# Kernel tuning notes

Measured on AMD Instinct MI355X. Metric: run time of the kernel, lower is better.

Reference implementation:

```python
import jax, jax.numpy as jnp
import numpy as np

T, B, D, H, S = 512, 32, 1024, 1024, 512


def setup_inputs() -> dict:
    key = jax.random.key(0)
    ks = jax.random.split(key, 10)
    sc = 0.02
    return {
        "x": jax.random.normal(ks[0], (T, B, D), jnp.float32),
        "h0": jax.random.normal(ks[1], (B, H), jnp.float32),
        "c0": jax.random.normal(ks[2], (B, H), jnp.float32),
        "ctx": jax.random.normal(ks[3], (S, B, H), jnp.float32),
        # nn.Linear(input_size, 4*hidden_size) with bias
        "W_ih": jax.random.normal(ks[4], (4 * H, D), jnp.float32) * sc,
        "b_ih": jax.random.normal(ks[5], (4 * H,), jnp.float32) * sc,
        # nn.Linear(hidden_size, 4*hidden_size) with bias
        "W_hh": jax.random.normal(ks[6], (4 * H, H), jnp.float32) * sc,
        "b_hh": jax.random.normal(ks[7], (4 * H,), jnp.float32) * sc,
        # SoftDotAttention: linear_in (H->H, no bias), linear_out (2H->H, no bias)
        "W_in": jax.random.normal(ks[8], (H, H), jnp.float32) * sc,
        "W_out": jax.random.normal(ks[9], (H, 2 * H), jnp.float32) * sc,
    }


def reference(x, h0, c0, ctx, W_ih, b_ih, W_hh, b_hh, W_in, W_out):
    ctx_b = jnp.swapaxes(ctx, 0, 1)  # [B, S, H] (ctx.transpose(0,1))

    def step(carry, xt):
        hx, cx = carry
        gates = xt @ W_ih.T + b_ih + hx @ W_hh.T + b_hh  # [B, 4H]
        i, f, g, o = jnp.split(gates, 4, axis=1)
        cy = jax.nn.sigmoid(f) * cx + jax.nn.sigmoid(i) * jnp.tanh(g)
        hy = jax.nn.sigmoid(o) * jnp.tanh(cy)  # [B, H]
        # SoftDotAttention
        target = hy @ W_in.T  # [B, H]
        attn = jax.nn.softmax(jnp.einsum("bsh,bh->bs", ctx_b, target), axis=-1)
        wc = jnp.einsum("bs,bsh->bh", attn, ctx_b)  # weighted context
        h_tilde = jnp.tanh(jnp.concatenate([wc, hy], axis=1) @ W_out.T)
        return (h_tilde, cy), h_tilde

    (hT, cT), out = jax.lax.scan(step, (h0, c0), x)
    return out, hT, cT
```

## Files before the change

### kernel.cpp

```cpp
#include <hip/hip_runtime.h>
#include <hip/hip_bf16.h>
#include <cstdint>
#include <cstddef>

#define TT 512
#define BB 32
#define DD 1024
#define HH 1024
#define SS 512

typedef _Float16 f16x8 __attribute__((ext_vector_type(8)));
typedef _Float16 f16x4 __attribute__((ext_vector_type(4)));
typedef _Float16 f16x2 __attribute__((ext_vector_type(2)));
typedef float f32x4 __attribute__((ext_vector_type(4)));

__device__ __forceinline__ float sigm(float x) { return 1.0f / (1.0f + __expf(-x)); }
__device__ __forceinline__ float tanh_fast(float x) {
    return 1.0f - 2.0f / (__expf(2.0f * x) + 1.0f);
}
__device__ __forceinline__ f16x8 cvt8(const float* __restrict__ p) {
    float4 u = *(const float4*)p;
    float4 v = *(const float4*)(p + 4);
    f16x8 r;
    r[0] = (_Float16)u.x; r[1] = (_Float16)u.y; r[2] = (_Float16)u.z; r[3] = (_Float16)u.w;
    r[4] = (_Float16)v.x; r[5] = (_Float16)v.y; r[6] = (_Float16)v.z; r[7] = (_Float16)v.w;
    return r;
}

__device__ __forceinline__ void st_u32_coh(unsigned* p, unsigned v) {
    __hip_atomic_store(p, v, __ATOMIC_RELAXED, __HIP_MEMORY_SCOPE_AGENT);
}
__device__ __forceinline__ unsigned ld_u32_coh(const unsigned* p) {
    return __hip_atomic_load(p, __ATOMIC_RELAXED, __HIP_MEMORY_SCOPE_AGENT);
}
__device__ __forceinline__ unsigned long long ld_u64_coh(const unsigned long long* p) {
    return __hip_atomic_load(p, __ATOMIC_RELAXED, __HIP_MEMORY_SCOPE_AGENT);
}
__device__ __forceinline__ f16x8 ld16_coh(const _Float16* p) {
    union { unsigned long long q[2]; f16x8 h; } u;
    u.q[0] = ld_u64_coh((const unsigned long long*)p);
    u.q[1] = ld_u64_coh((const unsigned long long*)p + 1);
    return u.h;
}

__global__ __launch_bounds__(256) void k_cvt(const float* __restrict__ s,
                                             _Float16* __restrict__ d, int n4) {
    for (int i = blockIdx.x * blockDim.x + threadIdx.x; i < n4; i += gridDim.x * blockDim.x) {
        float4 v = ((const float4*)s)[i];
        f16x4 h;
        h[0] = (_Float16)v.x; h[1] = (_Float16)v.y;
        h[2] = (_Float16)v.z; h[3] = (_Float16)v.w;
        ((f16x4*)d)[i] = h;
    }
}

__global__ void k_bias(const float* __restrict__ bih, const float* __restrict__ bhh,
                       float* __restrict__ bsum) {
    const int i = blockIdx.x * blockDim.x + threadIdx.x;
    if (i < 4 * HH) bsum[i] = bih[i] + bhh[i];
}

__global__ void k_init(const float* __restrict__ c0, float* __restrict__ cbuf) {
    const int i = blockIdx.x * blockDim.x + threadIdx.x;
    if (i < BB * HH) cbuf[i] = c0[i];
}

__global__ void k_zero(unsigned* __restrict__ p) {
    const int i = blockIdx.x * blockDim.x + threadIdx.x;
    if (i < 1024) p[i] = 0u;
}

__global__ void k_fin(const float* __restrict__ lasth, const float* __restrict__ cbuf,
                      float* __restrict__ hT, float* __restrict__ cT) {
    const int i = blockIdx.x * blockDim.x + threadIdx.x;
    if (i < BB * HH) {
        hT[i] = lasth[i];
        cT[i] = cbuf[i];
    }
}

__global__ __launch_bounds__(256) void k_pre(const float* __restrict__ x,
                                             const float* __restrict__ Wih,
                                             _Float16* __restrict__ gx) {
    const int wave = (blockIdx.x * blockDim.x + threadIdx.x) >> 6;
    const int lane = threadIdx.x & 63;
    const int m0 = (wave >> 6) * 64, n0 = (wave & 63) * 64;
    const int lm = lane & 15, q8 = (lane >> 4) * 8;

    f32x4 acc[4][4];
    #pragma unroll
    for (int i = 0; i < 4; ++i)
        #pragma unroll
        for (int j = 0; j < 4; ++j) acc[i][j] = (f32x4)0.0f;

    for (int k0 = 0; k0 < DD; k0 += 32) {
        f16x8 a[4], b[4];
        #pragma unroll
        for (int i = 0; i < 4; ++i)
            a[i] = cvt8(x + (size_t)(m0 + i * 16 + lm) * DD + k0 + q8);
        #pragma unroll
        for (int j = 0; j < 4; ++j)
            b[j] = cvt8(Wih + (size_t)(n0 + j * 16 + lm) * DD + k0 + q8);
        #pragma unroll
        for (int i = 0; i < 4; ++i)
            #pragma unroll
            for (int j = 0; j < 4; ++j)
                acc[i][j] = __builtin_amdgcn_mfma_f32_16x16x32_f16(a[i], b[j], acc[i][j], 0, 0, 0);
    }
    const int rq = (lane >> 4) * 4;
    #pragma unroll
    for (int i = 0; i < 4; ++i)
        #pragma unroll
        for (int j = 0; j < 4; ++j)
            #pragma unroll
            for (int r = 0; r < 4; ++r)
                gx[(size_t)(m0 + i * 16 + rq + r) * (4 * HH) + n0 + j * 16 + lm] =
                    (_Float16)acc[i][j][r];
}

__global__ __launch_bounds__(256) void k_trwin(const float* __restrict__ Win,
                                               _Float16* __restrict__ WinT) {
    __shared__ float tile[32][33];
    const int bx = blockIdx.x & 31, by = blockIdx.x >> 5;
    const int tx = threadIdx.x & 31, ty = threadIdx.x >> 5;
    #pragma unroll
    for (int r = 0; r < 4; ++r)
        tile[ty + r * 8][tx] = Win[(size_t)(by * 32 + ty + r * 8) * HH + bx * 32 + tx];
    __syncthreads();
    #pragma unroll
    for (int r = 0; r < 4; ++r)
        WinT[(size_t)(bx * 32 + ty + r * 8) * HH + by * 32 + tx] =
            (_Float16)tile[tx][ty + r * 8];
}

__global__ __launch_bounds__(256) void k_ctxw(const float* __restrict__ ctxf,
                                              const _Float16* __restrict__ WinT,
                                              _Float16* __restrict__ ctxW) {
    const int wave = (blockIdx.x * blockDim.x + threadIdx.x) >> 6;
    const int lane = threadIdx.x & 63;
    const int m0 = (wave >> 4) * 64, n0 = (wave & 15) * 64;
    const int lm = lane & 15, q8 = (lane >> 4) * 8;

    f32x4 acc[4][4];
    #pragma unroll
    for (int i = 0; i < 4; ++i)
        #pragma unroll
        for (int j = 0; j < 4; ++j) acc[i][j] = (f32x4)0.0f;

    for (int k0 = 0; k0 < HH; k0 += 32) {
        f16x8 a[4], b[4];
        #pragma unroll
        for (int i = 0; i < 4; ++i)
            a[i] = cvt8(ctxf + (size_t)(m0 + i * 16 + lm) * HH + k0 + q8);
        #pragma unroll
        for (int j = 0; j < 4; ++j)
            b[j] = *(const f16x8*)(WinT + (size_t)(n0 + j * 16 + lm) * HH + k0 + q8);
        #pragma unroll
        for (int i = 0; i < 4; ++i)
            #pragma unroll
            for (int j = 0; j < 4; ++j)
                acc[i][j] = __builtin_amdgcn_mfma_f32_16x16x32_f16(a[i], b[j], acc[i][j], 0, 0, 0);
    }
    const int rq = (lane >> 4) * 4;
    #pragma unroll
    for (int i = 0; i < 4; ++i)
        #pragma unroll
        for (int j = 0; j < 4; ++j)
            #pragma unroll
            for (int r = 0; r < 4; ++r)
                ctxW[(size_t)(m0 + i * 16 + rq + r) * HH + n0 + j * 16 + lm] =
                    (_Float16)acc[i][j][r];
}

__device__ __forceinline__ void gbar4(unsigned* __restrict__ flags, unsigned round) {
    __syncthreads();
    const int tid = threadIdx.x;
    if (tid == 0) {
        asm volatile("s_waitcnt vmcnt(0)" ::: "memory");
        st_u32_coh(&flags[blockIdx.x], round);
    }
    if (tid < 64) {
        int guard = 0;
        for (;;) {
            const unsigned a0 = ld_u32_coh(&flags[tid * 4 + 0]);
            const unsigned a1 = ld_u32_coh(&flags[tid * 4 + 1]);
            const unsigned a2 = ld_u32_coh(&flags[tid * 4 + 2]);
            const unsigned a3 = ld_u32_coh(&flags[tid * 4 + 3]);
            if (a0 >= round && a1 >= round && a2 >= round && a3 >= round) break;
            __builtin_amdgcn_s_sleep(1);
            if (++guard > (1 << 20)) break;
        }
    }
    __syncthreads();
}

__global__ __launch_bounds__(512, 1) void k_persist(
    const _Float16* __restrict__ x16,
    const _Float16* __restrict__ ctx_h,
    const _Float16* __restrict__ ctxW,
    const float* __restrict__ Whh,
    const float* __restrict__ Wih,
    const float* __restrict__ Wout,
    const float* __restrict__ bsum,
    const float* __restrict__ c0i,
    float* __restrict__ cbuf,
    _Float16* __restrict__ h16,
    _Float16* __restrict__ hy16,
    _Float16* __restrict__ wc16,
    float* __restrict__ scores,
    float* __restrict__ out,
    unsigned* __restrict__ bar) {
    __shared__ __align__(16) _Float16 sWHH[16 * 1024];
    __shared__ __align__(16) _Float16 sWIH[16 * 1024];
    __shared__ __align__(16) _Float16 sWOUT[4 * 2048];
    __shared__ __align__(16) _Float16 sH[32 * 1024];
    __shared__ __align__(16) float sRED[2048];
    __shared__ float sSM[512];
    __shared__ float sCB[128];

    const int bid = blockIdx.x;
    const int tid = threadIdx.x;
    const int w = tid >> 6, lane = tid & 63;
    const int lm = lane & 15, q8 = (lane >> 4) * 8;
    const int j0 = bid * 4;

    for (int idx = tid; idx < 16 * 128; idx += 512) {
        const int p = idx >> 7, k8 = idx & 127;
        const int g = (p >> 2) * HH + j0 + (p & 3);
        const int dst = (p * 2048 + k8 * 16) ^ ((p & 7) << 4);
        *(f16x8*)((char*)sWHH + dst) = cvt8(Whh + (size_t)g * HH + k8 * 8);
        *(f16x8*)((char*)sWIH + dst) = cvt8(Wih + (size_t)g * DD + k8 * 8);
    }
    for (int idx = tid; idx < 4 * 256; idx += 512) {
        const int p = idx >> 8, k8 = idx & 255;
        *(f16x8*)((char*)sWOUT + ((p * 4096 + k8 * 16) ^ (p << 4))) =
            cvt8(Wout + (size_t)(j0 + p) * (2 * HH) + k8 * 8);
    }
    if (tid < 128) sCB[tid] = c0i[(size_t)(tid >> 2) * HH + j0 + (tid & 3)];
    __syncthreads();

    unsigned round = 0;
    for (int t = 0; t < TT; ++t) {
        {
            #pragma unroll
            for (int u = 0; u < 8; ++u) {
                const int idx = u * 512 + tid;
                const int row = idx >> 7, c16 = idx & 127;
                const f16x8 v = ld16_coh(h16 + (size_t)row * HH + c16 * 8);
                *(f16x8*)((char*)sH + ((row * 2048 + c16 * 16) ^ ((row & 7) << 4))) = v;
            }
            __syncthreads();
            const int kb = (w & 3) * 256;
            f32x4 acc0 = (f32x4)0.0f, acc1 = (f32x4)0.0f;
            if (w < 4) {
                #pragma unroll
                for (int kk = 0; kk < 256; kk += 32) {
                    const int k0 = kb + kk + q8;
                    f16x8 a0 = *(const f16x8*)((const char*)sH +
                                 ((lm * 2048 + k0 * 2) ^ ((lm & 7) << 4)));
                    f16x8 a1 = *(const f16x8*)((const char*)sH +
                                 (((16 + lm) * 2048 + k0 * 2) ^ ((lm & 7) << 4)));
                    f16x8 bb = *(const f16x8*)((const char*)sWHH +
                                 ((lm * 2048 + k0 * 2) ^ ((lm & 7) << 4)));
                    acc0 = __builtin_amdgcn_mfma_f32_16x16x32_f16(a0, bb, acc0, 0, 0, 0);
                    acc1 = __builtin_amdgcn_mfma_f32_16x16x32_f16(a1, bb, acc1, 0, 0, 0);
                }
            } else {
                const _Float16* Xb = x16 + (size_t)t * (BB * DD);
                #pragma unroll
                for (int kk = 0; kk < 256; kk += 32) {
                    const int k0 = kb + kk + q8;
                    f16x8 a0 = *(const f16x8*)(Xb + (size_t)lm * DD + k0);
                    f16x8 a1 = *(const f16x8*)(Xb + (size_t)(16 + lm) * DD + k0);
                    f16x8 bb = *(const f16x8*)((const char*)sWIH +
                                 ((lm * 2048 + k0 * 2) ^ ((lm & 7) << 4)));
                    acc0 = __builtin_amdgcn_mfma_f32_16x16x32_f16(a0, bb, acc0, 0, 0, 0);
                    acc1 = __builtin_amdgcn_mfma_f32_16x16x32_f16(a1, bb, acc1, 0, 0, 0);
                }
            }
            ((f32x4*)sRED)[w * 64 + lane] = acc0;
            __syncthreads();
            if (tid < 256) {
                const int b = tid >> 4, p = tid & 15;
                const int bi = b & 15;
                const int ln = ((bi >> 2) << 4) | p, r = bi & 3;
                float gv = 0.0f;
                #pragma unroll
                for (int w2 = 0; w2 < 8; ++w2) gv += sRED[(w2 * 64 + ln) * 4 + r];
                sSM[tid] = gv;
            }
            __syncthreads();
            ((f32x4*)sRED)[w * 64 + lane] = acc1;
            __syncthreads();
            if (tid >= 256) {
                const int b = tid >> 4, p = tid & 15;
                const int bi = b & 15;
                const int ln = ((bi >> 2) << 4) | p, r = bi & 3;
                float gv = 0.0f;
                #pragma unroll
                for (int w2 = 0; w2 < 8; ++w2) gv += sRED[(w2 * 64 + ln) * 4 + r];
                sSM[tid] = gv;
            }
            __syncthreads();
            if (tid < 64) {
                const int b = tid >> 1, cp = (tid & 1) * 2;
                union { _Float16 h[2]; unsigned u; } pk;
                #pragma unroll
                for (int cc = 0; cc < 2; ++cc) {
                    const int c = cp + cc, j = j0 + c;
                    const float gi = sSM[b * 16 + 0 + c] + bsum[j];
                    const float gf = sSM[b * 16 + 4 + c] + bsum[HH + j];
                    const float gg = sSM[b * 16 + 8 + c] + bsum[2 * HH + j];
                    const float go = sSM[b * 16 + 12 + c] + bsum[3 * HH + j];
                    const float cprev = sCB[b * 4 + c];
                    const float cy = sigm(gf) * cprev + sigm(gi) * tanh_fast(gg);
                    const float hv = sigm(go) * tanh_fast(cy);
                    sCB[b * 4 + c] = cy;
                    pk.h[cc] = (_Float16)hv;
                }
                st_u32_coh((unsigned*)(hy16 + (size_t)b * HH + j0 + cp), pk.u);
            }
        }
        ++round;
        gbar4(bar, round);

        {
            const int b = bid & 31, s0 = (bid >> 5) * 64;
            const _Float16* hrow = hy16 + (size_t)b * HH + lane * 16;
            const f16x8 hv0 = ld16_coh(hrow);
            const f16x8 hv1 = ld16_coh(hrow + 8);
            float hf[16];
            #pragma unroll
            for (int i = 0; i < 8; ++i) { hf[i] = (float)hv0[i]; hf[8 + i] = (float)hv1[i]; }
            f16x8 cr0[8], cr1[8];
            #pragma unroll
            for (int i = 0; i < 8; ++i) {
                const _Float16* crow =
                    ctxW + ((size_t)(s0 + w * 8 + i) * BB + b) * HH + lane * 16;
                cr0[i] = *(const f16x8*)(crow);
                cr1[i] = *(const f16x8*)(crow + 8);
            }
            #pragma unroll
            for (int i = 0; i < 8; ++i) {
                float sum = 0.0f;
                #pragma unroll
                for (int jj = 0; jj < 8; ++jj)
                    sum += hf[jj] * (float)cr0[i][jj] + hf[8 + jj] * (float)cr1[i][jj];
                #pragma unroll
                for (int off = 32; off > 0; off >>= 1) sum += __shfl_down(sum, off, 64);
                if (lane == 0)
                    st_u32_coh((unsigned*)(scores + b * SS + s0 + w * 8 + i),
                               __float_as_uint(sum));
            }
        }
        ++round;
        gbar4(bar, round);

        {
            const int b = bid >> 3, h0 = (bid & 7) * 128;
            const float v =
                __uint_as_float(ld_u32_coh((const unsigned*)(scores + b * SS + tid)));
            float mx = v;
            #pragma unroll
            for (int off = 32; off > 0; off >>= 1) mx = fmaxf(mx, __shfl_xor(mx, off, 64));
            if (lane == 0) sRED[w] = mx;
            __syncthreads();
            mx = sRED[0];
            #pragma unroll
            for (int w2 = 1; w2 < 8; ++w2) mx = fmaxf(mx, sRED[w2]);
            const float e = __expf(v - mx);
            sSM[tid] = e;
            float ssum = e;
            #pragma unroll
            for (int off = 32; off > 0; off >>= 1) ssum += __shfl_xor(ssum, off, 64);
            if (lane == 0) sRED[8 + w] = ssum;
            __syncthreads();
            float tot = 0.0f;
            #pragma unroll
            for (int w2 = 0; w2 < 8; ++w2) tot += sRED[8 + w2];
            const float inv = 1.0f / tot;
            const int g = lane >> 4, c = lane & 15;
            float acc[8];
            #pragma unroll
            for (int jj = 0; jj < 8; ++jj) acc[jj] = 0.0f;
            const _Float16* cb =
                ctx_h + ((size_t)(w * 64 + g) * BB + b) * HH + h0 + c * 8;
            #pragma unroll
            for (int i = 0; i < 16; ++i) {
                const float aw = sSM[w * 64 + g + i * 4];
                const f16x8 u = *(const f16x8*)(cb + (size_t)(i * 4) * (BB * HH));
                #pragma unroll
                for (int jj = 0; jj < 8; ++jj) acc[jj] += aw * (float)u[jj];
            }
            #pragma unroll
            for (int jj = 0; jj < 8; ++jj) {
                acc[jj] += __shfl_xor(acc[jj], 16, 64);
                acc[jj] += __shfl_xor(acc[jj], 32, 64);
            }
            __syncthreads();
            if (g == 0) {
                #pragma unroll
                for (int jj = 0; jj < 8; ++jj) sRED[w * 128 + c * 8 + jj] = acc[jj];
            }
            __syncthreads();
            if (tid < 64) {
                const int ccol = tid * 2;
                float sv0 = 0.0f, sv1 = 0.0f;
                #pragma unroll
                for (int w2 = 0; w2 < 8; ++w2) {
                    sv0 += sRED[w2 * 128 + ccol];
                    sv1 += sRED[w2 * 128 + ccol + 1];
                }
                union { _Float16 h[2]; unsigned u; } pk;
                pk.h[0] = (_Float16)(sv0 * inv);
                pk.h[1] = (_Float16)(sv1 * inv);
                st_u32_coh((unsigned*)(wc16 + (size_t)b * HH + h0 + ccol), pk.u);
            }
        }
        ++round;
        gbar4(bar, round);

        {
            const int pc = lm & 3;
            const int kb = w * 128;
            f32x4 acc0 = (f32x4)0.0f, acc1 = (f32x4)0.0f;
            #pragma unroll
            for (int u = 0; u < 8; ++u) {
                const int idx = u * 512 + tid;
                const int row = idx >> 7, c16 = idx & 127;
                const f16x8 v = ld16_coh(wc16 + (size_t)row * HH + c16 * 8);
                *(f16x8*)((char*)sH + ((row * 2048 + c16 * 16) ^ ((row & 7) << 4))) = v;
            }
            __syncthreads();
            #pragma unroll
            for (int kk = 0; kk < 128; kk += 32) {
                const int k0 = kb + kk + q8;
                f16x8 a0 = *(const f16x8*)((const char*)sH +
                             ((lm * 2048 + k0 * 2) ^ ((lm & 7) << 4)));
                f16x8 a1 = *(const f16x8*)((const char*)sH +
                             (((16 + lm) * 2048 + k0 * 2) ^ ((lm & 7) << 4)));
                f16x8 bb = *(const f16x8*)((const char*)sWOUT +
                             ((pc * 4096 + k0 * 2) ^ (pc << 4)));
                acc0 = __builtin_amdgcn_mfma_f32_16x16x32_f16(a0, bb, acc0, 0, 0, 0);
                acc1 = __builtin_amdgcn_mfma_f32_16x16x32_f16(a1, bb, acc1, 0, 0, 0);
            }
            __syncthreads();
            #pragma unroll
            for (int u = 0; u < 8; ++u) {
                const int idx = u * 512 + tid;
                const int row = idx >> 7, c16 = idx & 127;
                const f16x8 v = ld16_coh(hy16 + (size_t)row * HH + c16 * 8);
                *(f16x8*)((char*)sH + ((row * 2048 + c16 * 16) ^ ((row & 7) << 4))) = v;
            }
            __syncthreads();
            #pragma unroll
            for (int kk = 0; kk < 128; kk += 32) {
                const int k0 = kb + kk + q8;
                f16x8 a0 = *(const f16x8*)((const char*)sH +
                             ((lm * 2048 + k0 * 2) ^ ((lm & 7) << 4)));
                f16x8 a1 = *(const f16x8*)((const char*)sH +
                             (((16 + lm) * 2048 + k0 * 2) ^ ((lm & 7) << 4)));
                f16x8 bb = *(const f16x8*)((const char*)sWOUT +
                             ((pc * 4096 + (HH + k0) * 2) ^ (pc << 4)));
                acc0 = __builtin_amdgcn_mfma_f32_16x16x32_f16(a0, bb, acc0, 0, 0, 0);
                acc1 = __builtin_amdgcn_mfma_f32_16x16x32_f16(a1, bb, acc1, 0, 0, 0);
            }
            ((f32x4*)sRED)[w * 64 + lane] = acc0;
            __syncthreads();
            if (tid < 256) {
                const int b = tid >> 4, p = tid & 15;
                const int bi = b & 15;
                const int ln = ((bi >> 2) << 4) | p, r = bi & 3;
                float v2 = 0.0f;
                #pragma unroll
                for (int w2 = 0; w2 < 8; ++w2) v2 += sRED[(w2 * 64 + ln) * 4 + r];
                const float ht = tanh_fast(v2);
                if (p < 4)
                    st_u32_coh((unsigned*)(out + (size_t)t * (BB * HH) + b * HH + j0 + p),
                               __float_as_uint(ht));
                sSM[tid] = ht;
            }
            __syncthreads();
            ((f32x4*)sRED)[w * 64 + lane] = acc1;
            __syncthreads();
            if (tid >= 256) {
                const int b = tid >> 4, p = tid & 15;
                const int bi = b & 15;
                const int ln = ((bi >> 2) << 4) | p, r = bi & 3;
                float v2 = 0.0f;
                #pragma unroll
                for (int w2 = 0; w2 < 8; ++w2) v2 += sRED[(w2 * 64 + ln) * 4 + r];
                const float ht = tanh_fast(v2);
                if (p < 4)
                    st_u32_coh((unsigned*)(out + (size_t)t * (BB * HH) + b * HH + j0 + p),
                               __float_as_uint(ht));
                sSM[tid] = ht;
            }
            __syncthreads();
            if (tid < 64) {
                const int b2 = tid >> 1, pp = (tid & 1) * 2;
                union { _Float16 h[2]; unsigned u; } pk;
                pk.h[0] = (_Float16)sSM[b2 * 16 + pp];
                pk.h[1] = (_Float16)sSM[b2 * 16 + pp + 1];
                st_u32_coh((unsigned*)(h16 + (size_t)b2 * HH + j0 + pp), pk.u);
            }
        }
        ++round;
        gbar4(bar, round);
    }

    if (tid < 128)
        st_u32_coh((unsigned*)&cbuf[(size_t)(tid >> 2) * HH + j0 + (tid & 3)],
                   __float_as_uint(sCB[tid]));
}

__global__ __launch_bounds__(64) void k_step1(const float* __restrict__ hprev,
                                              const _Float16* __restrict__ Whh_h,
                                              const float* __restrict__ Whh_f,
                                              const _Float16* __restrict__ gx_t,
                                              const float* __restrict__ xt_f,
                                              const _Float16* __restrict__ Wih_h,
                                              const float* __restrict__ Wih_f,
                                              const float* __restrict__ bsum,
                                              float* __restrict__ cbuf,
                                              float* __restrict__ hy,
                                              int use_pre, int staged) {
    const int wave = blockIdx.x;
    const int lane = threadIdx.x;
    const int m0 = (wave >> 6) * 16;
    const int j0 = (wave & 63) * 16;
    const int lm = lane & 15, q8 = (lane >> 4) * 8;

    f32x4 acc[4];
    #pragma unroll
    for (int q = 0; q < 4; ++q) acc[q] = (f32x4)0.0f;

    const float* arow = hprev + (size_t)(m0 + lm) * HH;
    if (staged) {
        for (int k0 = 0; k0 < HH; k0 += 32) {
            f16x8 a = cvt8(arow + k0 + q8);
            #pragma unroll
            for (int q = 0; q < 4; ++q) {
                f16x8 b = *(const f16x8*)(Whh_h + (size_t)(q * HH + j0 + lm) * HH + k0 + q8);
                acc[q] = __builtin_amdgcn_mfma_f32_16x16x32_f16(a, b, acc[q], 0, 0, 0);
            }
        }
    } else {
        for (int k0 = 0; k0 < HH; k0 += 32) {
            f16x8 a = cvt8(arow + k0 + q8);
            #pragma unroll
            for (int q = 0; q < 4; ++q) {
                f16x8 b = cvt8(Whh_f + (size_t)(q * HH + j0 + lm) * HH + k0 + q8);
                acc[q] = __builtin_amdgcn_mfma_f32_16x16x32_f16(a, b, acc[q], 0, 0, 0);
            }
        }
    }
    if (!use_pre) {
        const float* xrow = xt_f + (size_t)(m0 + lm) * DD;
        if (staged) {
            for (int k0 = 0; k0 < DD; k0 += 32) {
                f16x8 a = cvt8(xrow + k0 + q8);
                #pragma unroll
                for (int q = 0; q < 4; ++q) {
                    f16x8 b = *(const f16x8*)(Wih_h + (size_t)(q * HH + j0 + lm) * DD + k0 + q8);
                    acc[q] = __builtin_amdgcn_mfma_f32_16x16x32_f16(a, b, acc[q], 0, 0, 0);
                }
            }
        } else {
            for (int k0 = 0; k0 < DD; k0 += 32) {
                f16x8 a = cvt8(xrow + k0 + q8);
                #pragma unroll
                for (int q = 0; q < 4; ++q) {
                    f16x8 b = cvt8(Wih_f + (size_t)(q * HH + j0 + lm) * DD + k0 + q8);
                    acc[q] = __builtin_amdgcn_mfma_f32_16x16x32_f16(a, b, acc[q], 0, 0, 0);
                }
            }
        }
    }
    const int rq = (lane >> 4) * 4;
    const int j = j0 + lm;
    const float bs_i = bsum[j], bs_f = bsum[HH + j], bs_g = bsum[2 * HH + j], bs_o = bsum[3 * HH + j];
    #pragma unroll
    for (int r = 0; r < 4; ++r) {
        const int b = m0 + rq + r;
        float gi = acc[0][r] + bs_i, gf = acc[1][r] + bs_f;
        float gg = acc[2][r] + bs_g, go = acc[3][r] + bs_o;
        if (use_pre) {
            const _Float16* g = gx_t + (size_t)b * (4 * HH);
            gi += (float)g[j];
            gf += (float)g[HH + j];
            gg += (float)g[2 * HH + j];
            go += (float)g[3 * HH + j];
        }
        const float cprev = cbuf[b * HH + j];
        const float cy = sigm(gf) * cprev + sigm(gi) * tanh_fast(gg);
        const float hv = sigm(go) * tanh_fast(cy);
        cbuf[b * HH + j] = cy;
        hy[b * HH + j] = hv;
    }
}

__global__ __launch_bounds__(64) void k_target(const float* __restrict__ hy,
                                               const _Float16* __restrict__ Win_h,
                                               const float* __restrict__ Win_f,
                                               float* __restrict__ target,
                                               int staged) {
    const int wave = blockIdx.x;
    const int lane = threadIdx.x;
    const int m0 = (wave >> 6) * 16;
    const int j0 = (wave & 63) * 16;
    const int lm = lane & 15, q8 = (lane >> 4) * 8;

    f32x4 acc = (f32x4)0.0f;
    const float* arow = hy + (size_t)(m0 + lm) * HH;
    if (staged) {
        for (int k0 = 0; k0 < HH; k0 += 32) {
            f16x8 a = cvt8(arow + k0 + q8);
            f16x8 b = *(const f16x8*)(Win_h + (size_t)(j0 + lm) * HH + k0 + q8);
            acc = __builtin_amdgcn_mfma_f32_16x16x32_f16(a, b, acc, 0, 0, 0);
        }
    } else {
        for (int k0 = 0; k0 < HH; k0 += 32) {
            f16x8 a = cvt8(arow + k0 + q8);
            f16x8 b = cvt8(Win_f + (size_t)(j0 + lm) * HH + k0 + q8);
            acc = __builtin_amdgcn_mfma_f32_16x16x32_f16(a, b, acc, 0, 0, 0);
        }
    }
    const int rq = (lane >> 4) * 4;
    const int j = j0 + lm;
    #pragma unroll
    for (int r = 0; r < 4; ++r)
        target[(m0 + rq + r) * HH + j] = acc[r];
}

__global__ __launch_bounds__(256) void k_scores(const _Float16* __restrict__ ctx_h,
                                                const float* __restrict__ ctx_f,
                                                const float* __restrict__ target,
                                                float* __restrict__ scores, int staged) {
    const int idx = (blockIdx.x * blockDim.x + threadIdx.x) >> 6;
    const int lane = threadIdx.x & 63;
    const int b = idx >> 9;
    const int s = idx & 511;
    const float* trow = target + b * HH + lane * 16;
    float4 t0 = *(const float4*)(trow);
    float4 t1 = *(const float4*)(trow + 4);
    float4 t2 = *(const float4*)(trow + 8);
    float4 t3 = *(const float4*)(trow + 12);
    float sum = 0.0f;
    if (staged) {
        const _Float16* crow = ctx_h + ((size_t)s * BB + b) * HH + lane * 16;
        f16x8 c0 = *(const f16x8*)(crow);
        f16x8 c1 = *(const f16x8*)(crow + 8);
        sum += (float)c0[0] * t0.x + (float)c0[1] * t0.y + (float)c0[2] * t0.z + (float)c0[3] * t0.w;
        sum += (float)c0[4] * t1.x + (float)c0[5] * t1.y + (float)c0[6] * t1.z + (float)c0[7] * t1.w;
        sum += (float)c1[0] * t2.x + (float)c1[1] * t2.y + (float)c1[2] * t2.z + (float)c1[3] * t2.w;
        sum += (float)c1[4] * t3.x + (float)c1[5] * t3.y + (float)c1[6] * t3.z + (float)c1[7] * t3.w;
    } else {
        const float* crow = ctx_f + ((size_t)s * BB + b) * HH + lane * 16;
        float4 c0 = *(const float4*)(crow);
        float4 c1 = *(const float4*)(crow + 4);
        float4 c2 = *(const float4*)(crow + 8);
        float4 c3 = *(const float4*)(crow + 12);
        sum += c0.x * t0.x + c0.y * t0.y + c0.z * t0.z + c0.w * t0.w;
        sum += c1.x * t1.x + c1.y * t1.y + c1.z * t1.z + c1.w * t1.w;
        sum += c2.x * t2.x + c2.y * t2.y + c2.z * t2.z + c2.w * t2.w;
        sum += c3.x * t3.x + c3.y * t3.y + c3.z * t3.z + c3.w * t3.w;
    }
    #pragma unroll
    for (int off = 32; off > 0; off >>= 1) sum += __shfl_down(sum, off, 64);
    if (lane == 0) scores[b * SS + s] = sum;
}

__global__ __launch_bounds__(256) void k_attn(const _Float16* __restrict__ ctx_h,
                                              const float* __restrict__ ctx_f,
                                              const float* __restrict__ scores,
                                              float* __restrict__ wc, int staged) {
    __shared__ float sm[SS];
    __shared__ float red[256];
    const int b = blockIdx.x >> 1;
    const int hc = blockIdx.x & 1;
    const int t = threadIdx.x;

    const float v0 = scores[b * SS + t];
    const float v1 = scores[b * SS + 256 + t];
    red[t] = fmaxf(v0, v1);
    __syncthreads();
    for (int o = 128; o > 0; o >>= 1) {
        if (t < o) red[t] = fmaxf(red[t], red[t + o]);
        __syncthreads();
    }
    const float mx = red[0];
    __syncthreads();
    const float e0 = __expf(v0 - mx);
    const float e1 = __expf(v1 - mx);
    sm[t] = e0;
    sm[t + 256] = e1;
    red[t] = e0 + e1;
    __syncthreads();
    for (int o = 128; o > 0; o >>= 1) {
        if (t < o) red[t] += red[t + o];
        __syncthreads();
    }
    const float inv = 1.0f / red[0];

    const int h = hc * 512 + t * 2;
    float a0 = 0.0f, a1 = 0.0f;
    if (staged) {
        const _Float16* cbase = ctx_h + (size_t)b * HH + h;
        #pragma unroll 8
        for (int s = 0; s < SS; ++s) {
            const float a = sm[s];
            const f16x2 u = *(const f16x2*)(cbase + (size_t)s * (BB * HH));
            a0 += a * (float)u[0];
            a1 += a * (float)u[1];
        }
    } else {
        const float* cbase = ctx_f + (size_t)b * HH + h;
        #pragma unroll 8
        for (int s = 0; s < SS; ++s) {
            const float a = sm[s];
            const float2 u = *(const float2*)(cbase + (size_t)s * (BB * HH));
            a0 += a * u.x;
            a1 += a * u.y;
        }
    }
    wc[b * HH + h] = a0 * inv;
    wc[b * HH + h + 1] = a1 * inv;
}

__global__ __launch_bounds__(64) void k_out(const float* __restrict__ wc,
                                            const float* __restrict__ hy,
                                            const _Float16* __restrict__ Wout_h,
                                            const float* __restrict__ Wout_f,
                                            float* __restrict__ out_t,
                                            int staged) {
    const int wave = blockIdx.x;
    const int lane = threadIdx.x;
    const int m0 = (wave >> 6) * 16;
    const int j0 = (wave & 63) * 16;
    const int lm = lane & 15, q8 = (lane >> 4) * 8;

    f32x4 acc = (f32x4)0.0f;
    const float* arow1 = wc + (size_t)(m0 + lm) * HH;
    const float* arow2 = hy + (size_t)(m0 + lm) * HH;
    if (staged) {
        const _Float16* brow = Wout_h + (size_t)(j0 + lm) * (2 * HH);
        for (int k0 = 0; k0 < HH; k0 += 32) {
            f16x8 a = cvt8(arow1 + k0 + q8);
            f16x8 b = *(const f16x8*)(brow + k0 + q8);
            acc = __builtin_amdgcn_mfma_f32_16x16x32_f16(a, b, acc, 0, 0, 0);
        }
        for (int k0 = 0; k0 < HH; k0 += 32) {
            f16x8 a = cvt8(arow2 + k0 + q8);
            f16x8 b = *(const f16x8*)(brow + HH + k0 + q8);
            acc = __builtin_amdgcn_mfma_f32_16x16x32_f16(a, b, acc, 0, 0, 0);
        }
    } else {
        const float* brow = Wout_f + (size_t)(j0 + lm) * (2 * HH);
        for (int k0 = 0; k0 < HH; k0 += 32) {
            f16x8 a = cvt8(arow1 + k0 + q8);
            f16x8 b = cvt8(brow + k0 + q8);
            acc = __builtin_amdgcn_mfma_f32_16x16x32_f16(a, b, acc, 0, 0, 0);
        }
        for (int k0 = 0; k0 < HH; k0 += 32) {
            f16x8 a = cvt8(arow2 + k0 + q8);
            f16x8 b = cvt8(brow + HH + k0 + q8);
            acc = __builtin_amdgcn_mfma_f32_16x16x32_f16(a, b, acc, 0, 0, 0);
        }
    }
    const int rq = (lane >> 4) * 4;
    const int j = j0 + lm;
    #pragma unroll
    for (int r = 0; r < 4; ++r)
        out_t[(m0 + rq + r) * HH + j] = tanh_fast(acc[r]);
}

static constexpr size_t NW_CBUF   = 0;
static constexpr size_t NW_SCORES = 131072;
static constexpr size_t NW_HY16   = 196608;
static constexpr size_t NW_H16    = 262144;
static constexpr size_t NW_WC16   = 327680;
static constexpr size_t NW_BSUM   = 393216;
static constexpr size_t NW_BAR    = 409600;
static constexpr size_t NW_WINT   = 413696;
static constexpr size_t NW_X16    = 2510848;
static constexpr size_t NW_CTXH   = 36065280;
static constexpr size_t NW_CTXW   = 69619712;
static constexpr size_t NW_TOTAL  = 103174144;

extern "C" void kernel_launch(void* const* d_in, const int* in_sizes, int n_in,
                              void* d_out, int out_size, void* d_ws, size_t ws_size,
                              hipStream_t stream) {
    const float* x    = (const float*)d_in[0];
    const float* h0   = (const float*)d_in[1];
    const float* c0   = (const float*)d_in[2];
    const float* ctx  = (const float*)d_in[3];
    const float* Wih  = (const float*)d_in[4];
    const float* bih  = (const float*)d_in[5];
    const float* Whh  = (const float*)d_in[6];
    const float* bhh  = (const float*)d_in[7];
    const float* Win  = (const float*)d_in[8];
    const float* Wout = (const float*)d_in[9];
    float* out = (float*)d_out;
    char* ws = (char*)d_ws;

    if (ws_size >= NW_TOTAL) {
        float* cbuf       = (float*)(ws + NW_CBUF);
        float* scores     = (float*)(ws + NW_SCORES);
        _Float16* hy16    = (_Float16*)(ws + NW_HY16);
        _Float16* h16     = (_Float16*)(ws + NW_H16);
        _Float16* wc16    = (_Float16*)(ws + NW_WC16);
        float* bsum       = (float*)(ws + NW_BSUM);
        unsigned* bar     = (unsigned*)(ws + NW_BAR);
        _Float16* WinT    = (_Float16*)(ws + NW_WINT);
        _Float16* x16     = (_Float16*)(ws + NW_X16);
        _Float16* ctx_h   = (_Float16*)(ws + NW_CTXH);
        _Float16* ctxW    = (_Float16*)(ws + NW_CTXW);

        k_bias<<<16, 256, 0, stream>>>(bih, bhh, bsum);
        k_zero<<<4, 256, 0, stream>>>(bar);
        k_cvt<<<2048, 256, 0, stream>>>(ctx, ctx_h, SS * BB * HH / 4);
        k_cvt<<<4096, 256, 0, stream>>>(x, x16, TT * BB * DD / 4);
        k_cvt<<<32, 256, 0, stream>>>(h0, h16, BB * HH / 4);
        k_trwin<<<1024, 256, 0, stream>>>(Win, WinT);
        k_ctxw<<<1024, 256, 0, stream>>>(ctx, WinT, ctxW);

        k_persist<<<256, 512, 0, stream>>>(x16, ctx_h, ctxW, Whh, Wih, Wout, bsum,
                                           c0, cbuf, h16, hy16, wc16, scores, out, bar);

        float* hT = out + (size_t)TT * BB * HH;
        float* cT = hT + BB * HH;
        k_fin<<<128, 256, 0, stream>>>(out + (size_t)(TT - 1) * BB * HH, cbuf, hT, cT);
        return;
    }

    float* cbuf   = (float*)(ws + 0);
    float* hy     = (float*)(ws + 131072);
    float* target = (float*)(ws + 262144);
    float* scores = (float*)(ws + 393216);
    float* wc     = (float*)(ws + 458752);
    float* bsum   = (float*)(ws + 589824);
    _Float16* Whh_h  = (_Float16*)(ws + 606208);
    _Float16* Win_h  = (_Float16*)(ws + 8994816);
    _Float16* Wout_h = (_Float16*)(ws + 11091968);
    _Float16* Wih_h  = (_Float16*)(ws + 15286272);
    _Float16* ctx_h  = (_Float16*)(ws + 23674880);
    _Float16* gx     = (_Float16*)(ws + 57229312);

    const int staged  = (ws_size >= (size_t)57229312) ? 1 : 0;
    const int use_pre = (ws_size >= (size_t)191447040) ? 1 : 0;

    k_bias<<<16, 256, 0, stream>>>(bih, bhh, bsum);
    k_init<<<128, 256, 0, stream>>>(c0, cbuf);
    if (staged) {
        k_cvt<<<1024, 256, 0, stream>>>(Whh, Whh_h, 4 * HH * HH / 4);
        k_cvt<<<1024, 256, 0, stream>>>(Win, Win_h, HH * HH / 4);
        k_cvt<<<1024, 256, 0, stream>>>(Wout, Wout_h, 2 * HH * HH / 4);
        k_cvt<<<2048, 256, 0, stream>>>(ctx, ctx_h, SS * BB * HH / 4);
        if (!use_pre) k_cvt<<<1024, 256, 0, stream>>>(Wih, Wih_h, 4 * HH * DD / 4);
    }
    if (use_pre) k_pre<<<4096, 256, 0, stream>>>(x, Wih, gx);

    for (int t = 0; t < TT; ++t) {
        const float* hprev = (t == 0) ? h0 : (out + (size_t)(t - 1) * BB * HH);
        const _Float16* gx_t = gx + (size_t)t * BB * 4 * HH;
        const float* xt = x + (size_t)t * BB * DD;
        float* out_t = out + (size_t)t * BB * HH;

        k_step1<<<128, 64, 0, stream>>>(hprev, Whh_h, Whh, gx_t, xt, Wih_h, Wih,
                                        bsum, cbuf, hy, use_pre, staged);
        k_target<<<128, 64, 0, stream>>>(hy, Win_h, Win, target, staged);
        k_scores<<<4096, 256, 0, stream>>>(ctx_h, ctx, target, scores, staged);
        k_attn<<<64, 256, 0, stream>>>(ctx_h, ctx, scores, wc, staged);
        k_out<<<128, 64, 0, stream>>>(wc, hy, Wout_h, Wout, out_t, staged);
    }

    float* hT = out + (size_t)TT * BB * HH;
    float* cT = hT + BB * HH;
    k_fin<<<128, 256, 0, stream>>>(out + (size_t)(TT - 1) * BB * HH, cbuf, hT, cT);
}
```

Before: 24.88 ms.

## Use per-timestep ring buffers so cross-block exchanges can use plain cached loads

Adds per-timestep ring buffers for the hy and weighted-context exchanges. Each step then writes to fresh addresses, so readers switch from relaxed agent-scope atomic loads to ordinary vector loads. The recurrent h is read straight from the fp32 output of the previous step and converted to fp16, which removes the separate h16 store. This costs about 67 MB more workspace and twice the bytes on the h read. The path only runs when the workspace is large enough, and it relies on no stale cached lines existing at the fresh ring addresses.

```diff
diff --git a/kernel.cpp b/kernel.cpp
--- a/kernel.cpp
+++ b/kernel.cpp
@@ -41,6 +41,9 @@
     u.q[0] = ld_u64_coh((const unsigned long long*)p);
     u.q[1] = ld_u64_coh((const unsigned long long*)p + 1);
     return u.h;
+}
+__device__ __forceinline__ f16x8 ld16_mix(const _Float16* p, bool coh) {
+    return coh ? ld16_coh(p) : *(const f16x8*)p;
 }
 
 __global__ __launch_bounds__(256) void k_cvt(const float* __restrict__ s,
@@ -202,14 +205,18 @@
     const float* __restrict__ Wih,
     const float* __restrict__ Wout,
     const float* __restrict__ bsum,
+    const float* __restrict__ h0f,
     const float* __restrict__ c0i,
     float* __restrict__ cbuf,
     _Float16* __restrict__ h16,
     _Float16* __restrict__ hy16,
     _Float16* __restrict__ wc16,
+    _Float16* __restrict__ hyring,
+    _Float16* __restrict__ wcring,
     float* __restrict__ scores,
     float* __restrict__ out,
-    unsigned* __restrict__ bar) {
+    unsigned* __restrict__ bar,
+    int use_ring) {
     __shared__ __align__(16) _Float16 sWHH[16 * 1024];
     __shared__ __align__(16) _Float16 sWIH[16 * 1024];
     __shared__ __align__(16) _Float16 sWOUT[4 * 2048];
@@ -223,6 +230,7 @@
     const int w = tid >> 6, lane = tid & 63;
     const int lm = lane & 15, q8 = (lane >> 4) * 8;
     const int j0 = bid * 4;
+    const bool coh = !use_ring;
 
     for (int idx = tid; idx < 16 * 128; idx += 512) {
         const int p = idx >> 7, k8 = idx & 127;
@@ -241,13 +249,27 @@
 
     unsigned round = 0;
     for (int t = 0; t < TT; ++t) {
+        _Float16* hyb = use_ring ? (hyring + (size_t)t * (BB * HH)) : hy16;
+        _Float16* wcb = use_ring ? (wcring + (size_t)t * (BB * HH)) : wc16;
+
         {
-            #pragma unroll
-            for (int u = 0; u < 8; ++u) {
-                const int idx = u * 512 + tid;
-                const int row = idx >> 7, c16 = idx & 127;
-                const f16x8 v = ld16_coh(h16 + (size_t)row * HH + c16 * 8);
-                *(f16x8*)((char*)sH + ((row * 2048 + c16 * 16) ^ ((row & 7) << 4))) = v;
+            if (use_ring) {
+                const float* hsrc = (t == 0) ? h0f : (out + (size_t)(t - 1) * (BB * HH));
+                #pragma unroll
+                for (int u = 0; u < 8; ++u) {
+                    const int idx = u * 512 + tid;
+                    const int row = idx >> 7, c16 = idx & 127;
+                    const f16x8 v = cvt8(hsrc + (size_t)row * HH + c16 * 8);
+                    *(f16x8*)((char*)sH + ((row * 2048 + c16 * 16) ^ ((row & 7) << 4))) = v;
+                }
+            } else {
+                #pragma unroll
+                for (int u = 0; u < 8; ++u) {
+                    const int idx = u * 512 + tid;
+                    const int row = idx >> 7, c16 = idx & 127;
+                    const f16x8 v = ld16_coh(h16 + (size_t)row * HH + c16 * 8);
+                    *(f16x8*)((char*)sH + ((row * 2048 + c16 * 16) ^ ((row & 7) << 4))) = v;
+                }
             }
             __syncthreads();
             const int kb = (w & 3) * 256;
@@ -318,7 +340,7 @@
                     sCB[b * 4 + c] = cy;
                     pk.h[cc] = (_Float16)hv;
                 }
-                st_u32_coh((unsigned*)(hy16 + (size_t)b * HH + j0 + cp), pk.u);
+                st_u32_coh((unsigned*)(hyb + (size_t)b * HH + j0 + cp), pk.u);
             }
         }
         ++round;
@@ -326,9 +348,9 @@
 
         {
             const int b = bid & 31, s0 = (bid >> 5) * 64;
-            const _Float16* hrow = hy16 + (size_t)b * HH + lane * 16;
-            const f16x8 hv0 = ld16_coh(hrow);
-            const f16x8 hv1 = ld16_coh(hrow + 8);
+            const _Float16* hrow = hyb + (size_t)b * HH + lane * 16;
+            const f16x8 hv0 = ld16_mix(hrow, coh);
+            const f16x8 hv1 = ld16_mix(hrow + 8, coh);
             float hf[16];
             #pragma unroll
             for (int i = 0; i < 8; ++i) { hf[i] = (float)hv0[i]; hf[8 + i] = (float)hv1[i]; }
@@ -414,7 +436,7 @@
                 union { _Float16 h[2]; unsigned u; } pk;
                 pk.h[0] = (_Float16)(sv0 * inv);
                 pk.h[1] = (_Float16)(sv1 * inv);
-                st_u32_coh((unsigned*)(wc16 + (size_t)b * HH + h0 + ccol), pk.u);
+                st_u32_coh((unsigned*)(wcb + (size_t)b * HH + h0 + ccol), pk.u);
             }
         }
         ++round;
@@ -428,7 +450,7 @@
             for (int u = 0; u < 8; ++u) {
                 const int idx = u * 512 + tid;
                 const int row = idx >> 7, c16 = idx & 127;
-                const f16x8 v = ld16_coh(wc16 + (size_t)row * HH + c16 * 8);
+                const f16x8 v = ld16_mix(wcb + (size_t)row * HH + c16 * 8, coh);
                 *(f16x8*)((char*)sH + ((row * 2048 + c16 * 16) ^ ((row & 7) << 4))) = v;
             }
             __syncthreads();
@@ -449,7 +471,7 @@
             for (int u = 0; u < 8; ++u) {
                 const int idx = u * 512 + tid;
                 const int row = idx >> 7, c16 = idx & 127;
-                const f16x8 v = ld16_coh(hy16 + (size_t)row * HH + c16 * 8);
+                const f16x8 v = ld16_mix(hyb + (size_t)row * HH + c16 * 8, coh);
                 *(f16x8*)((char*)sH + ((row * 2048 + c16 * 16) ^ ((row & 7) << 4))) = v;
             }
             __syncthreads();
@@ -497,7 +519,7 @@
                 sSM[tid] = ht;
             }
             __syncthreads();
-            if (tid < 64) {
+            if (!use_ring && tid < 64) {
                 const int b2 = tid >> 1, pp = (tid & 1) * 2;
                 union { _Float16 h[2]; unsigned u; } pk;
                 pk.h[0] = (_Float16)sSM[b2 * 16 + pp];
@@ -787,6 +809,9 @@
 static constexpr size_t NW_CTXH   = 36065280;
 static constexpr size_t NW_CTXW   = 69619712;
 static constexpr size_t NW_TOTAL  = 103174144;
+static constexpr size_t NW_HYRING = 103174144;
+static constexpr size_t NW_WCRING = 136728576;
+static constexpr size_t NW_RING_TOTAL = 170283008;
 
 extern "C" void kernel_launch(void* const* d_in, const int* in_sizes, int n_in,
                               void* d_out, int out_size, void* d_ws, size_t ws_size,
@@ -816,6 +841,9 @@
         _Float16* x16     = (_Float16*)(ws + NW_X16);
         _Float16* ctx_h   = (_Float16*)(ws + NW_CTXH);
         _Float16* ctxW    = (_Float16*)(ws + NW_CTXW);
+        const int use_ring = (ws_size >= NW_RING_TOTAL) ? 1 : 0;
+        _Float16* hyring  = (_Float16*)(ws + NW_HYRING);
+        _Float16* wcring  = (_Float16*)(ws + NW_WCRING);
 
         k_bias<<<16, 256, 0, stream>>>(bih, bhh, bsum);
         k_zero<<<4, 256, 0, stream>>>(bar);
@@ -826,7 +854,8 @@
         k_ctxw<<<1024, 256, 0, stream>>>(ctx, WinT, ctxW);
 
         k_persist<<<256, 512, 0, stream>>>(x16, ctx_h, ctxW, Whh, Wih, Wout, bsum,
-                                           c0, cbuf, h16, hy16, wc16, scores, out, bar);
+                                           h0, c0, cbuf, h16, hy16, wc16,
+                                           hyring, wcring, scores, out, bar, use_ring);
 
         float* hT = out + (size_t)TT * BB * HH;
         float* cT = hT + BB * HH;
```

Measured after the change: 22.06 ms. -11.3%, faster.
